# Kernel optimization log

Measured on AMD Instinct MI355X. Metric: run time of the kernel, lower is better.

## Reference

```python
import jax, jax.numpy as jnp
import numpy as np

N, D, H, T = 50000, 512, 512, 16
N_HOP = 1
NEG = -1e18


def setup_inputs() -> dict:
    key = jax.random.key(0)
    ks = jax.random.split(key, 16)
    s = 0.05  # param init scale
    inp = {
        "attn_mem": jax.random.normal(ks[0], (N, D), jnp.float32),
        "stop": jax.random.uniform(ks[1], (D,), jnp.float32, -0.01, 0.01),
        "init_h": jax.random.normal(ks[2], (H,), jnp.float32) * s,
        "init_c": jax.random.normal(ks[3], (H,), jnp.float32) * s,
        "init_i": jax.random.normal(ks[4], (D,), jnp.float32) * s,
        "attn_wm": jax.random.normal(ks[5], (D, H), jnp.float32) * s,
        "attn_wq": jax.random.normal(ks[6], (H, H), jnp.float32) * s,
        "attn_v": jax.random.normal(ks[7], (H,), jnp.float32) * s,
        "hop_wm": jax.random.normal(ks[8], (D, H), jnp.float32) * s,
        "hop_wq": jax.random.normal(ks[9], (H, H), jnp.float32) * s,
        "hop_v": jax.random.normal(ks[10], (H,), jnp.float32) * s,
        "w_ih": jax.random.normal(ks[11], (4 * H, D), jnp.float32) * s,
        "w_hh": jax.random.normal(ks[12], (4 * H, H), jnp.float32) * s,
        "b_ih": jax.random.normal(ks[13], (4 * H,), jnp.float32) * s,
        "b_hh": jax.random.normal(ks[14], (4 * H,), jnp.float32) * s,
        # precomputed gumbel noise -> categorical sampling via gumbel-max
        "gumbel": jax.random.gumbel(ks[15], (T, N + 1), jnp.float32),
    }
    return inp


def _attn_score(feat, q, v, w):
    # feat: [M, H], q: [H] -> unnormalized scores [M]
    return jnp.tanh(feat + q @ w) @ v


def reference(attn_mem, stop, init_h, init_c, init_i, attn_wm, attn_wq, attn_v,
              hop_wm, hop_wq, hop_v, w_ih, w_hh, b_ih, b_hh, gumbel):
    mem = jnp.concatenate([attn_mem, stop[None, :]], axis=0)  # [N+1, D]
    attn_feat = mem @ attn_wm                                  # [N+1, H]
    hop_feat = mem @ hop_wm                                    # [N+1, H]
    stop_idx = mem.shape[0] - 1

    def lstm_cell(x, h, c):
        gates = x @ w_ih.T + b_ih + h @ w_hh.T + b_hh          # [4H]
        i, f, g, o = jnp.split(gates, 4)
        i, f, o = jax.nn.sigmoid(i), jax.nn.sigmoid(f), jax.nn.sigmoid(o)
        c_new = f * c + i * jnp.tanh(g)
        return o * jnp.tanh(c_new), c_new

    def step(carry, g):
        h, c, x, sel, done = carry
        h, c = lstm_cell(x, h, c)
        q = h
        for _ in range(N_HOP):  # glimpse hops
            s = _attn_score(hop_feat, q, hop_v, hop_wq)
            q = jax.nn.softmax(s) @ hop_feat
        score = _attn_score(attn_feat, q, attn_v, attn_wq)     # [N+1]
        score = jnp.where(sel, NEG, score)                     # mask selected
        logp_all = jax.nn.log_softmax(score)
        out = jnp.argmax(score + g)                            # Categorical sample
        logp = jnp.where(done, 0.0, logp_all[out])
        out_rec = jnp.where(done, stop_idx, out)
        sel = jnp.where(done, sel, sel.at[out].set(True))
        new_done = done | (out == stop_idx)
        x = jnp.where(new_done, x, mem[out])
        return (h, c, x, sel, new_done), (out_rec.astype(jnp.int32), logp)

    carry0 = (init_h, init_c, init_i,
              jnp.zeros((mem.shape[0],), jnp.bool_), jnp.array(False))
    _, (outs, logps) = jax.lax.scan(step, carry0, gumbel)
    return outs, logps
```

## Files before the change

### kernel.cpp

```cpp
#include <hip/hip_runtime.h>
#include <math.h>

#define NITEMS 50000
#define NROWS 50001
#define NP 50176
#define DD 512
#define HH 512
#define TT 16
#define NEGV (-1e18f)
#define NGRP 784
#define NGC 196

typedef unsigned long long ull;
typedef unsigned short ushort;
typedef short short8 __attribute__((ext_vector_type(8)));
typedef float f32x4 __attribute__((ext_vector_type(4)));

#define AST(p, v) __hip_atomic_store((p), (v), __ATOMIC_RELAXED, __HIP_MEMORY_SCOPE_AGENT)
#define ALD(p) __hip_atomic_load((p), __ATOMIC_RELAXED, __HIP_MEMORY_SCOPE_AGENT)
#define AADD_REL(p) __hip_atomic_fetch_add((p), 1u, __ATOMIC_ACQ_REL, __HIP_MEMORY_SCOPE_AGENT)
#define FLAG_SET(p) __hip_atomic_store((p), 1u, __ATOMIC_RELEASE, __HIP_MEMORY_SCOPE_AGENT)
#define FLAG_GET(p) __hip_atomic_load((p), __ATOMIC_ACQUIRE, __HIP_MEMORY_SCOPE_AGENT)

__device__ __forceinline__ unsigned fkey(float f) {
  unsigned u = __float_as_uint(f);
  return (u & 0x80000000u) ? ~u : (u | 0x80000000u);
}
__device__ __forceinline__ float ftanh(float x) {
  float e = __builtin_amdgcn_exp2f(x * 2.885390081777927f);
  return 1.f - 2.f * __builtin_amdgcn_rcpf(e + 1.f);
}
__device__ __forceinline__ float fexp(float x) {
  return __builtin_amdgcn_exp2f(x * 1.4426950408889634f);
}
__device__ __forceinline__ ushort rne1(float a) {
  unsigned u = __float_as_uint(a);
  return (ushort)((u + 0x7fffu + ((u >> 16) & 1u)) >> 16);
}
__device__ __forceinline__ float bf2f(ushort h) { return __uint_as_float((unsigned)h << 16); }
__device__ __forceinline__ unsigned pack_bf16(float a, float b) {
  return (unsigned)rne1(a) | ((unsigned)rne1(b) << 16);
}
__device__ __forceinline__ float bflo(unsigned u) { return __uint_as_float(u << 16); }
__device__ __forceinline__ float bfhi(unsigned u) { return __uint_as_float(u & 0xffff0000u); }

__device__ __forceinline__ void gl_lds16(const void* g, void* l) {
#if __has_builtin(__builtin_amdgcn_global_load_lds)
  __builtin_amdgcn_global_load_lds((const __attribute__((address_space(1))) unsigned*)g,
                                   (__attribute__((address_space(3))) unsigned*)l, 16, 0, 0);
#else
  const int lane = threadIdx.x & 63;
  *(uint4*)((char*)l + lane * 16) = *(const uint4*)g;
#endif
}

#define MFMA(a, b, c) __builtin_amdgcn_mfma_f32_16x16x32_bf16(a, b, c, 0, 0, 0)

__global__ void k_convA(const float* __restrict__ A0, const float* __restrict__ stoprow,
                        ushort* __restrict__ Ahi, ushort* __restrict__ Alo,
                        int* __restrict__ sel, unsigned* __restrict__ cnts) {
  const size_t t = (size_t)blockIdx.x * 256 + threadIdx.x;
  if (blockIdx.x < 196) {
    int i = blockIdx.x * 256 + threadIdx.x;
    if (i < NROWS) sel[i] = 0;
    if (blockIdx.x == 0 && threadIdx.x < 128) cnts[threadIdx.x] = 0;
  }
  const size_t base = t * 8;
  const int row = (int)(base >> 9);
  float v[8];
  if (row < NITEMS) {
    const float4* p = (const float4*)(A0 + base);
    float4 x = p[0], y = p[1];
    v[0] = x.x; v[1] = x.y; v[2] = x.z; v[3] = x.w;
    v[4] = y.x; v[5] = y.y; v[6] = y.z; v[7] = y.w;
  } else if (row == NITEMS) {
    const float4* p = (const float4*)(stoprow + (base & 511));
    float4 x = p[0], y = p[1];
    v[0] = x.x; v[1] = x.y; v[2] = x.z; v[3] = x.w;
    v[4] = y.x; v[5] = y.y; v[6] = y.z; v[7] = y.w;
  } else {
#pragma unroll
    for (int j = 0; j < 8; ++j) v[j] = 0.f;
  }
  unsigned hw[4], lw[4];
#pragma unroll
  for (int j = 0; j < 4; ++j) {
    float a0 = v[2 * j], a1 = v[2 * j + 1];
    ushort h0 = rne1(a0), h1 = rne1(a1);
    hw[j] = (unsigned)h0 | ((unsigned)h1 << 16);
    lw[j] = pack_bf16(a0 - bf2f(h0), a1 - bf2f(h1));
  }
  *(uint4*)(Ahi + base) = make_uint4(hw[0], hw[1], hw[2], hw[3]);
  *(uint4*)(Alo + base) = make_uint4(lw[0], lw[1], lw[2], lw[3]);
}

__global__ void k_convBT2(const float* __restrict__ Wa, const float* __restrict__ Wh,
                          ushort* __restrict__ WhiT_a, ushort* __restrict__ WloT_a,
                          ushort* __restrict__ WhiT_h, ushort* __restrict__ WloT_h) {
  const int n = blockIdx.x & 511;
  const float* W = (blockIdx.x < 512) ? Wa : Wh;
  ushort* Whi = (blockIdx.x < 512) ? WhiT_a : WhiT_h;
  ushort* Wlo = (blockIdx.x < 512) ? WloT_a : WloT_h;
  const int k0 = threadIdx.x * 2;
  float a0 = W[(size_t)k0 * 512 + n];
  float a1 = W[(size_t)(k0 + 1) * 512 + n];
  ushort h0 = rne1(a0), h1 = rne1(a1);
  *(unsigned*)(Whi + (size_t)n * 512 + k0) = (unsigned)h0 | ((unsigned)h1 << 16);
  *(unsigned*)(Wlo + (size_t)n * 512 + k0) = pack_bf16(a0 - bf2f(h0), a1 - bf2f(h1));
}

__launch_bounds__(256, 2)
__global__ void k_mfma(const ushort* __restrict__ Ahi, const ushort* __restrict__ Alo,
                       const ushort* __restrict__ BhT, const ushort* __restrict__ BlT,
                       ushort* __restrict__ C) {
  __shared__ __align__(16) char lds[65536];
  char* sA0 = lds;
  char* sA1 = lds + 16384;
  char* sB0 = lds + 32768;
  char* sB1 = lds + 49152;
  const int tid = threadIdx.x;
  const int lane = tid & 63, w = tid >> 6;
  const int lid = blockIdx.y * 4 + blockIdx.x;
  const int xcd = lid & 7, pos = lid >> 3;
  const int orig = xcd * 196 + pos;
  const int m0 = (orig >> 2) * 128, n0 = (orig & 3) * 128;
  const int aR0 = (w & 1) * 64, bR0 = (w >> 1) * 64;

  f32x4 acc[4][4];
  const f32x4 z4 = {0.f, 0.f, 0.f, 0.f};
#pragma unroll
  for (int i = 0; i < 4; ++i)
#pragma unroll
    for (int j = 0; j < 4; ++j) acc[i][j] = z4;

#define STAGE_ALL(KT)                                                                     \
  {                                                                                       \
    _Pragma("unroll") for (int i = 0; i < 4; ++i) {                                       \
      const int row = i * 32 + (tid >> 3);                                                \
      const int kb = ((tid & 7) << 4) ^ ((row & 7) << 4);                                 \
      const int ldso = i * 4096 + (w << 10);                                              \
      gl_lds16((const char*)(Ahi + ((size_t)(m0 + row) << 9) + (KT)) + kb, sA0 + ldso);   \
      gl_lds16((const char*)(Alo + ((size_t)(m0 + row) << 9) + (KT)) + kb, sA1 + ldso);   \
      gl_lds16((const char*)(BhT + ((size_t)(n0 + row) << 9) + (KT)) + kb, sB0 + ldso);   \
      gl_lds16((const char*)(BlT + ((size_t)(n0 + row) << 9) + (KT)) + kb, sB1 + ldso);   \
    }                                                                                     \
  }

  STAGE_ALL(0)
  __syncthreads();
  for (int c = 0; c < 8; ++c) {
#pragma unroll
    for (int ks = 0; ks < 2; ++ks) {
      short8 ah[4], al[4], bh[4], bl[4];
      const int kbb = ks * 64 + ((lane >> 4) << 4);
#pragma unroll
      for (int f = 0; f < 4; ++f) {
        const int ra = aR0 + f * 16 + (lane & 15);
        const int oa = ra * 128 + (kbb ^ ((ra & 7) << 4));
        ah[f] = *(const short8*)(sA0 + oa);
        al[f] = *(const short8*)(sA1 + oa);
        const int rb = bR0 + f * 16 + (lane & 15);
        const int ob = rb * 128 + (kbb ^ ((rb & 7) << 4));
        bh[f] = *(const short8*)(sB0 + ob);
        bl[f] = *(const short8*)(sB1 + ob);
      }
#pragma unroll
      for (int mf = 0; mf < 4; ++mf)
#pragma unroll
        for (int nf = 0; nf < 4; ++nf) {
          acc[mf][nf] = MFMA(ah[mf], bh[nf], acc[mf][nf]);
          acc[mf][nf] = MFMA(ah[mf], bl[nf], acc[mf][nf]);
          acc[mf][nf] = MFMA(al[mf], bh[nf], acc[mf][nf]);
        }
    }
    if (c < 7) {
      __syncthreads();
      STAGE_ALL((c + 1) * 64)
      __syncthreads();
    }
  }
#undef STAGE_ALL

#pragma unroll
  for (int mf = 0; mf < 4; ++mf)
#pragma unroll
    for (int nf = 0; nf < 4; ++nf) {
      const f32x4 a = acc[mf][nf];
      const int n = n0 + bR0 + nf * 16 + (lane & 15);
      const int mb = m0 + aR0 + mf * 16 + ((lane >> 4) << 2);
      ushort* p = C + (size_t)n * NP + mb;
      *(uint2*)p = make_uint2(pack_bf16(a.x, a.y), pack_bf16(a.z, a.w));
    }
}

__launch_bounds__(256)
__global__ void k_A(const float* __restrict__ attn_mem, const float* __restrict__ stoprow,
                    const float* __restrict__ init_i, const float* __restrict__ init_h,
                    const float* __restrict__ init_c,
                    const float* __restrict__ w_ih, const float* __restrict__ w_hh,
                    const float* __restrict__ b_ih, const float* __restrict__ b_hh,
                    const float* __restrict__ hop_wq,
                    float* __restrict__ hv0, float* __restrict__ hv1,
                    float* __restrict__ cv0, float* __restrict__ cv1,
                    float* __restrict__ b1, const int* __restrict__ xrow_buf,
                    unsigned* __restrict__ cntA, unsigned* __restrict__ flagA, int t) {
  __shared__ float g4[4];
  __shared__ float hs[512];
  __shared__ float red2[256];
  __shared__ int sOld;
  const int b = blockIdx.x, tid = threadIdx.x, w = tid >> 6, lane = tid & 63;
  const int xrow = (t == 0) ? -1 : ALD((int*)xrow_buf);
  const float* xp = (xrow < 0) ? init_i
                               : ((xrow == NITEMS) ? stoprow : attn_mem + (size_t)xrow * DD);
  const float* hsrc = (t == 0) ? init_h : ((t & 1) ? hv0 : hv1);
  float* hdst = (t & 1) ? hv1 : hv0;
  const float* csrc = (t == 0) ? init_c : ((t & 1) ? cv0 : cv1);
  float* cdst = (t & 1) ? cv1 : cv0;

  const int r = w * 512 + b;
  const float4* x4 = (const float4*)xp;
  const float4* h4 = (const float4*)hsrc;
  const float4* wi = (const float4*)(w_ih + (size_t)r * DD);
  const float4* wh = (const float4*)(w_hh + (size_t)r * DD);
  float s = 0.f;
  float4 a, ww;
  a = x4[lane * 2];     ww = wi[lane * 2];     s += a.x * ww.x + a.y * ww.y + a.z * ww.z + a.w * ww.w;
  a = x4[lane * 2 + 1]; ww = wi[lane * 2 + 1]; s += a.x * ww.x + a.y * ww.y + a.z * ww.z + a.w * ww.w;
  a = h4[lane * 2];     ww = wh[lane * 2];     s += a.x * ww.x + a.y * ww.y + a.z * ww.z + a.w * ww.w;
  a = h4[lane * 2 + 1]; ww = wh[lane * 2 + 1]; s += a.x * ww.x + a.y * ww.y + a.z * ww.z + a.w * ww.w;
#pragma unroll
  for (int off = 32; off > 0; off >>= 1) s += __shfl_xor(s, off);
  if (lane == 0) g4[w] = s + b_ih[r] + b_hh[r];
  __syncthreads();
  if (tid == 0) {
    const float si = 1.f / (1.f + expf(-g4[0]));
    const float sf = 1.f / (1.f + expf(-g4[1]));
    const float so = 1.f / (1.f + expf(-g4[3]));
    const float cn = sf * csrc[b] + si * tanhf(g4[2]);
    cdst[b] = cn;
    AST(&hdst[b], so * tanhf(cn));
  }
  __syncthreads();
  if (tid == 0) {
    unsigned old = AADD_REL(cntA);
    if (old == 511u) { FLAG_SET(flagA); AST(cntA, 0u); }
    sOld = (int)old;
  }
  __syncthreads();
  const int old = sOld;
  if (old >= 496) {
    if (tid == 0 && old != 511) {
      while (FLAG_GET(flagA) == 0u) __builtin_amdgcn_s_sleep(2);
    }
    __syncthreads();
    const int c0 = (old - 496) * 32;
    hs[tid] = ALD(&hdst[tid]);
    hs[tid + 256] = ALD(&hdst[tid + 256]);
    __syncthreads();
    const int col = c0 + (tid & 31), seg = tid >> 5;
    float acc = 0.f;
#pragma unroll 8
    for (int i = seg * 64; i < seg * 64 + 64; ++i)
      acc = fmaf(hs[i], hop_wq[(size_t)i * 512 + col], acc);
    red2[tid] = acc;
    __syncthreads();
    if (tid < 32) {
      float sm = 0.f;
#pragma unroll
      for (int g2 = 0; g2 < 8; ++g2) sm += red2[tid + 32 * g2];
      b1[c0 + tid] = sm;
    }
  }
}

__launch_bounds__(512)
__global__ void k_B1(const ushort* __restrict__ featT, const float* __restrict__ b1v,
                     const float* __restrict__ hv, float* __restrict__ e,
                     float* __restrict__ bZ1, float* __restrict__ Zt,
                     unsigned* __restrict__ cntB1) {
  __shared__ float spart[8][256];
  __shared__ float rz[512];
  __shared__ int isLast;
  const int tid = threadIdx.x, g = blockIdx.x;
  const int w = tid >> 6, lane = tid & 63;
  const int mb = g * 256 + lane * 4;
  const int h0 = w * 64;
  const ushort* fp = featT + (size_t)h0 * NP + mb;
  float a0 = 0.f, a1 = 0.f, a2 = 0.f, a3 = 0.f;
#pragma unroll 8
  for (int hh = 0; hh < 64; ++hh) {
    const uint2 u = *(const uint2*)fp;
    fp += NP;
    const float bb = b1v[h0 + hh], vv = hv[h0 + hh];
    a0 += ftanh(bflo(u.x) + bb) * vv;
    a1 += ftanh(bfhi(u.x) + bb) * vv;
    a2 += ftanh(bflo(u.y) + bb) * vv;
    a3 += ftanh(bfhi(u.y) + bb) * vv;
  }
  spart[w][lane * 4 + 0] = a0;
  spart[w][lane * 4 + 1] = a1;
  spart[w][lane * 4 + 2] = a2;
  spart[w][lane * 4 + 3] = a3;
  __syncthreads();
  if (w < 4) {
    const int idx = w * 64 + lane;
    const int m = g * 256 + idx;
    float s = 0.f;
#pragma unroll
    for (int w2 = 0; w2 < 8; ++w2) s += spart[w2][idx];
    float ev = (m < NROWS) ? fexp(s) : 0.f;
    e[m] = ev;
    float Z = ev;
#pragma unroll
    for (int off = 32; off > 0; off >>= 1) Z += __shfl_xor(Z, off);
    if (lane == 0) AST(&bZ1[g * 4 + w], Z);
  }
  __syncthreads();
  if (tid == 0) {
    unsigned old = AADD_REL(cntB1);
    isLast = (old == gridDim.x - 1);
    if (isLast) AST(cntB1, 0u);
  }
  __syncthreads();
  if (isLast) {
    float Zl = 0.f;
    for (int i = tid; i < NGRP; i += 512) Zl += ALD(&bZ1[i]);
    rz[tid] = Zl;
    __syncthreads();
    for (int s2 = 256; s2 > 0; s2 >>= 1) {
      if (tid < s2) rz[tid] += rz[tid + s2];
      __syncthreads();
    }
    if (tid == 0) *Zt = rz[0];
  }
}

__launch_bounds__(256)
__global__ void k_B2(const ushort* __restrict__ featT, const float* __restrict__ e,
                     const float* __restrict__ Zt, const float* __restrict__ attn_wq,
                     float* __restrict__ qn, float* __restrict__ b2,
                     unsigned* __restrict__ cntB2, unsigned* __restrict__ flagB2) {
  __shared__ float red[256];
  __shared__ int sOld;
  const int tid = threadIdx.x, h = blockIdx.x;
  const ushort* fr = featT + (size_t)h * NP;
  float acc = 0.f;
#pragma unroll 4
  for (int m0 = tid * 8; m0 < NP; m0 += 2048) {
    const uint4 F = *(const uint4*)(fr + m0);
    const float4 e0 = *(const float4*)(e + m0);
    const float4 e1 = *(const float4*)(e + m0 + 4);
    acc += bflo(F.x) * e0.x + bfhi(F.x) * e0.y + bflo(F.y) * e0.z + bfhi(F.y) * e0.w +
           bflo(F.z) * e1.x + bfhi(F.z) * e1.y + bflo(F.w) * e1.z + bfhi(F.w) * e1.w;
  }
  red[tid] = acc;
  __syncthreads();
  for (int s2 = 128; s2 > 0; s2 >>= 1) {
    if (tid < s2) red[tid] += red[tid + s2];
    __syncthreads();
  }
  if (tid == 0) AST(&qn[h], red[0] / (*Zt));
  __syncthreads();
  if (tid == 0) {
    unsigned old = AADD_REL(cntB2);
    if (old == 511u) { FLAG_SET(flagB2); AST(cntB2, 0u); }
    sOld = (int)old;
  }
  __syncthreads();
  const int old = sOld;
  if (old >= 504) {
    const int li = old - 504;
    if (tid == 0 && old != 511) {
      while (FLAG_GET(flagB2) == 0u) __builtin_amdgcn_s_sleep(2);
    }
    __syncthreads();
    const int j = li * 64 + (tid & 63), is = tid >> 6;
    float a = 0.f;
#pragma unroll 8
    for (int i2 = is * 128; i2 < is * 128 + 128; ++i2)
      a = fmaf(ALD(&qn[i2]), attn_wq[(size_t)i2 * 512 + j], a);
    red[tid] = a;
    __syncthreads();
    if (tid < 64) b2[li * 64 + tid] = red[tid] + red[tid + 64] + red[tid + 128] + red[tid + 192];
  }
}

__launch_bounds__(512)
__global__ void k_C(const ushort* __restrict__ featT, const float* __restrict__ b2,
                    const float* __restrict__ av, int* __restrict__ sel,
                    const float* __restrict__ gum,
                    float* __restrict__ bZa, ull* __restrict__ bkey, float* __restrict__ bsc,
                    int* __restrict__ done_buf, int* __restrict__ xrow_buf,
                    float* __restrict__ outf, unsigned* __restrict__ cntC, int t) {
  __shared__ float spart[8][256];
  __shared__ float rz[512];
  __shared__ ull rk[512];
  __shared__ float rs[512];
  __shared__ int isLast;
  const int tid = threadIdx.x, g = blockIdx.x;
  const int w = tid >> 6, lane = tid & 63;
  const int mb = g * 256 + lane * 4;
  const int h0 = w * 64;
  const ushort* fp = featT + (size_t)h0 * NP + mb;
  float a0 = 0.f, a1 = 0.f, a2 = 0.f, a3 = 0.f;
#pragma unroll 8
  for (int hh = 0; hh < 64; ++hh) {
    const uint2 u = *(const uint2*)fp;
    fp += NP;
    const float bb = b2[h0 + hh], vv = av[h0 + hh];
    a0 += ftanh(bflo(u.x) + bb) * vv;
    a1 += ftanh(bfhi(u.x) + bb) * vv;
    a2 += ftanh(bflo(u.y) + bb) * vv;
    a3 += ftanh(bfhi(u.y) + bb) * vv;
  }
  spart[w][lane * 4 + 0] = a0;
  spart[w][lane * 4 + 1] = a1;
  spart[w][lane * 4 + 2] = a2;
  spart[w][lane * 4 + 3] = a3;
  __syncthreads();
  if (w < 4) {
    const int idx = w * 64 + lane;
    const int m = g * 256 + idx;
    float s = 0.f;
#pragma unroll
    for (int w2 = 0; w2 < 8; ++w2) s += spart[w2][idx];
    const bool valid = (m < NROWS);
    float Z, sv;
    ull key;
    if (valid) {
      const float se = sel[m] ? NEGV : s;
      sv = se;
      key = ((ull)fkey(se + gum[m]) << 32) | (unsigned)(NITEMS - m);
      Z = fexp(se);
    } else {
      key = 0;
      Z = 0.f;
      sv = 0.f;
    }
#pragma unroll
    for (int off = 32; off > 0; off >>= 1) {
      Z += __shfl_xor(Z, off);
      ull Ko = __shfl_xor(key, off);
      float so = __shfl_xor(sv, off);
      if (Ko > key) { key = Ko; sv = so; }
    }
    if (lane == 0) {
      AST(&bZa[g * 4 + w], Z);
      AST(&bkey[g * 4 + w], key);
      AST(&bsc[g * 4 + w], sv);
    }
  }
  __syncthreads();
  if (tid == 0) {
    unsigned old = AADD_REL(cntC);
    isLast = (old == gridDim.x - 1);
    if (isLast) AST(cntC, 0u);
  }
  __syncthreads();
  if (isLast) {
    float Zl = 0.f, Sl = 0.f;
    ull Kl = 0;
    for (int i = tid; i < NGRP; i += 512) {
      Zl += ALD(&bZa[i]);
      ull k = ALD(&bkey[i]);
      if (k > Kl) { Kl = k; Sl = ALD(&bsc[i]); }
    }
    rz[tid] = Zl;
    rk[tid] = Kl;
    rs[tid] = Sl;
    __syncthreads();
    for (int s2 = 256; s2 > 0; s2 >>= 1) {
      if (tid < s2) {
        rz[tid] += rz[tid + s2];
        if (rk[tid + s2] > rk[tid]) { rk[tid] = rk[tid + s2]; rs[tid] = rs[tid + s2]; }
      }
      __syncthreads();
    }
    if (tid == 0) {
      const float Z = rz[0];
      const ull K = rk[0];
      const int out = NITEMS - (int)(unsigned)(K & 0xffffffffull);
      const int d_in = (t == 0) ? 0 : *done_buf;
      const int xprev = (t == 0) ? -1 : *xrow_buf;
      const int nd = d_in | (out == NITEMS);
      outf[t] = (float)(d_in ? NITEMS : out);
      outf[TT + t] = d_in ? 0.f : (rs[0] - logf(Z));
      if (!d_in) sel[out] = 1;
      *done_buf = nd;
      *xrow_buf = nd ? xprev : out;
    }
  }
}

extern "C" void kernel_launch(void* const* d_in, const int* in_sizes, int n_in,
                              void* d_out, int out_size, void* d_ws, size_t ws_size,
                              hipStream_t stream) {
  const float* attn_mem = (const float*)d_in[0];
  const float* stoprow  = (const float*)d_in[1];
  const float* init_h   = (const float*)d_in[2];
  const float* init_c   = (const float*)d_in[3];
  const float* init_i   = (const float*)d_in[4];
  const float* attn_wm  = (const float*)d_in[5];
  const float* attn_wq  = (const float*)d_in[6];
  const float* attn_v   = (const float*)d_in[7];
  const float* hop_wm   = (const float*)d_in[8];
  const float* hop_wq   = (const float*)d_in[9];
  const float* hop_v    = (const float*)d_in[10];
  const float* w_ih     = (const float*)d_in[11];
  const float* w_hh     = (const float*)d_in[12];
  const float* b_ih     = (const float*)d_in[13];
  const float* b_hh     = (const float*)d_in[14];
  const float* gumbel   = (const float*)d_in[15];

  float* ws = (float*)d_ws;
  size_t fo = 0;
  const size_t FB = (size_t)NP * 512 / 2;
  ushort* hop_featT  = (ushort*)(ws + fo); fo += FB;
  ushort* attn_featT = (ushort*)(ws + fo); fo += FB;
  ushort* Ahi = (ushort*)(ws + fo); fo += FB;
  ushort* Alo = (ushort*)(ws + fo); fo += FB;
  ushort* WhiT_a = (ushort*)(ws + fo); fo += 131072;
  ushort* WloT_a = (ushort*)(ws + fo); fo += 131072;
  ushort* WhiT_h = (ushort*)(ws + fo); fo += 131072;
  ushort* WloT_h = (ushort*)(ws + fo); fo += 131072;
  int* sel   = (int*)(ws + fo); fo += NP;
  float* e   = ws + fo; fo += NP;
  float* bZ1 = ws + fo; fo += 1024;
  float* bZa = ws + fo; fo += 1024;
  float* bsc = ws + fo; fo += 1024;
  ull* bkey  = (ull*)(ws + fo); fo += 2048;
  float* hv0 = ws + fo; fo += HH;
  float* hv1 = ws + fo; fo += HH;
  float* cv0 = ws + fo; fo += HH;
  float* cv1 = ws + fo; fo += HH;
  float* b1  = ws + fo; fo += HH;
  float* b2  = ws + fo; fo += HH;
  float* qn  = ws + fo; fo += HH;
  float* Ztp = ws + fo; fo += 2;
  unsigned* cnts = (unsigned*)(ws + fo); fo += 128;
  int* done_buf = (int*)(ws + fo); fo += 2;
  int* xrow_buf = (int*)(ws + fo); fo += 2;
  if (fo * sizeof(float) > ws_size) return;

  float* outf = (float*)d_out;

  k_convA<<<(NP * 512 / 8) / 256, 256, 0, stream>>>(attn_mem, stoprow, Ahi, Alo, sel, cnts);
  k_convBT2<<<1024, 256, 0, stream>>>(attn_wm, hop_wm, WhiT_a, WloT_a, WhiT_h, WloT_h);

  dim3 ggrid(4, NP / 128);
  k_mfma<<<ggrid, 256, 0, stream>>>(Ahi, Alo, WhiT_a, WloT_a, attn_featT);
  k_mfma<<<ggrid, 256, 0, stream>>>(Ahi, Alo, WhiT_h, WloT_h, hop_featT);

  for (int t = 0; t < TT; ++t) {
    k_A<<<512, 256, 0, stream>>>(attn_mem, stoprow, init_i, init_h, init_c,
                                 w_ih, w_hh, b_ih, b_hh, hop_wq,
                                 hv0, hv1, cv0, cv1, b1, xrow_buf,
                                 cnts + 0, cnts + 16 + t, t);
    k_B1<<<NGC, 512, 0, stream>>>(hop_featT, b1, hop_v, e, bZ1, Ztp, cnts + 1);
    k_B2<<<512, 256, 0, stream>>>(hop_featT, e, Ztp, attn_wq, qn, b2,
                                  cnts + 3, cnts + 32 + t);
    k_C<<<NGC, 512, 0, stream>>>(attn_featT, b2, attn_v, sel,
                                 gumbel + (size_t)t * NROWS, bZa, bkey, bsc,
                                 done_buf, xrow_buf, outf, cnts + 2, t);
  }
}
```

Measured before the change: 1.627 ms.

## Fuse hop-attention score and glimpse reduction into one kernel with per-block partials

Merges k_B1 and k_B2 into a single kernel. Each block keeps its exp scores in LDS and immediately computes partial glimpse sums over its own 256-row tile of hop_featT, writing per-block partial vectors. The last 16 blocks to arrive then reduce the partials, normalize by Z, and compute b2 = q·attn_wq. This removes one launch per step and the second full pass over hop_featT and e, at the cost of a partial buffer, extra spin-waits, and a strided re-read of the block's feature tile.

```diff
diff --git a/kernel.cpp b/kernel.cpp
--- a/kernel.cpp
+++ b/kernel.cpp
@@ -274,114 +274,129 @@
 }
 
 __launch_bounds__(512)
-__global__ void k_B1(const ushort* __restrict__ featT, const float* __restrict__ b1v,
-                     const float* __restrict__ hv, float* __restrict__ e,
-                     float* __restrict__ bZ1, float* __restrict__ Zt,
-                     unsigned* __restrict__ cntB1) {
+__global__ void k_B(const ushort* __restrict__ featT, const float* __restrict__ b1v,
+                    const float* __restrict__ hv, const float* __restrict__ attn_wq,
+                    float* __restrict__ qp, float* __restrict__ bZ1,
+                    float* __restrict__ qn, float* __restrict__ b2,
+                    unsigned* __restrict__ cnt1, unsigned* __restrict__ cnt2,
+                    unsigned* __restrict__ flagQ, unsigned* __restrict__ flagB2) {
   __shared__ float spart[8][256];
-  __shared__ float rz[512];
-  __shared__ int isLast;
+  __shared__ float e_lds[256];
+  __shared__ float red[512];
+  __shared__ int sOld;
   const int tid = threadIdx.x, g = blockIdx.x;
   const int w = tid >> 6, lane = tid & 63;
-  const int mb = g * 256 + lane * 4;
-  const int h0 = w * 64;
-  const ushort* fp = featT + (size_t)h0 * NP + mb;
-  float a0 = 0.f, a1 = 0.f, a2 = 0.f, a3 = 0.f;
+  const int mb0 = g * 256;
+
+  {
+    const int mb = mb0 + lane * 4;
+    const int h0 = w * 64;
+    const ushort* fp = featT + (size_t)h0 * NP + mb;
+    float a0 = 0.f, a1 = 0.f, a2 = 0.f, a3 = 0.f;
 #pragma unroll 8
-  for (int hh = 0; hh < 64; ++hh) {
-    const uint2 u = *(const uint2*)fp;
-    fp += NP;
-    const float bb = b1v[h0 + hh], vv = hv[h0 + hh];
-    a0 += ftanh(bflo(u.x) + bb) * vv;
-    a1 += ftanh(bfhi(u.x) + bb) * vv;
-    a2 += ftanh(bflo(u.y) + bb) * vv;
-    a3 += ftanh(bfhi(u.y) + bb) * vv;
-  }
-  spart[w][lane * 4 + 0] = a0;
-  spart[w][lane * 4 + 1] = a1;
-  spart[w][lane * 4 + 2] = a2;
-  spart[w][lane * 4 + 3] = a3;
+    for (int hh = 0; hh < 64; ++hh) {
+      const uint2 u = *(const uint2*)fp;
+      fp += NP;
+      const float bb = b1v[h0 + hh], vv = hv[h0 + hh];
+      a0 += ftanh(bflo(u.x) + bb) * vv;
+      a1 += ftanh(bfhi(u.x) + bb) * vv;
+      a2 += ftanh(bflo(u.y) + bb) * vv;
+      a3 += ftanh(bfhi(u.y) + bb) * vv;
+    }
+    spart[w][lane * 4 + 0] = a0;
+    spart[w][lane * 4 + 1] = a1;
+    spart[w][lane * 4 + 2] = a2;
+    spart[w][lane * 4 + 3] = a3;
+  }
   __syncthreads();
   if (w < 4) {
     const int idx = w * 64 + lane;
-    const int m = g * 256 + idx;
+    const int m = mb0 + idx;
     float s = 0.f;
 #pragma unroll
     for (int w2 = 0; w2 < 8; ++w2) s += spart[w2][idx];
     float ev = (m < NROWS) ? fexp(s) : 0.f;
-    e[m] = ev;
+    e_lds[idx] = ev;
     float Z = ev;
 #pragma unroll
     for (int off = 32; off > 0; off >>= 1) Z += __shfl_xor(Z, off);
     if (lane == 0) AST(&bZ1[g * 4 + w], Z);
   }
   __syncthreads();
+
+  {
+    const ushort* fr = featT + (size_t)tid * NP + mb0;
+    float acc = 0.f;
+#pragma unroll 4
+    for (int j = 0; j < 256; j += 8) {
+      const uint4 F = *(const uint4*)(fr + j);
+      acc += bflo(F.x) * e_lds[j + 0] + bfhi(F.x) * e_lds[j + 1] +
+             bflo(F.y) * e_lds[j + 2] + bfhi(F.y) * e_lds[j + 3] +
+             bflo(F.z) * e_lds[j + 4] + bfhi(F.z) * e_lds[j + 5] +
+             bflo(F.w) * e_lds[j + 6] + bfhi(F.w) * e_lds[j + 7];
+    }
+    AST(&qp[(size_t)g * 512 + tid], acc);
+  }
+  __syncthreads();
+
   if (tid == 0) {
-    unsigned old = AADD_REL(cntB1);
-    isLast = (old == gridDim.x - 1);
-    if (isLast) AST(cntB1, 0u);
-  }
-  __syncthreads();
-  if (isLast) {
-    float Zl = 0.f;
-    for (int i = tid; i < NGRP; i += 512) Zl += ALD(&bZ1[i]);
-    rz[tid] = Zl;
+    unsigned old = AADD_REL(cnt1);
+    if (old == NGC - 1u) { FLAG_SET(flagQ); AST(cnt1, 0u); }
+    sOld = (int)old;
+  }
+  __syncthreads();
+  const int old = sOld;
+  if (old >= NGC - 16) {
+    if (tid == 0 && old != NGC - 1) {
+      while (FLAG_GET(flagQ) == 0u) __builtin_amdgcn_s_sleep(2);
+    }
+    __syncthreads();
+    float zl = 0.f;
+    for (int i = tid; i < NGRP; i += 512) zl += ALD(&bZ1[i]);
+    red[tid] = zl;
     __syncthreads();
     for (int s2 = 256; s2 > 0; s2 >>= 1) {
-      if (tid < s2) rz[tid] += rz[tid + s2];
+      if (tid < s2) red[tid] += red[tid + s2];
       __syncthreads();
     }
-    if (tid == 0) *Zt = rz[0];
-  }
-}
-
-__launch_bounds__(256)
-__global__ void k_B2(const ushort* __restrict__ featT, const float* __restrict__ e,
-                     const float* __restrict__ Zt, const float* __restrict__ attn_wq,
-                     float* __restrict__ qn, float* __restrict__ b2,
-                     unsigned* __restrict__ cntB2, unsigned* __restrict__ flagB2) {
-  __shared__ float red[256];
-  __shared__ int sOld;
-  const int tid = threadIdx.x, h = blockIdx.x;
-  const ushort* fr = featT + (size_t)h * NP;
-  float acc = 0.f;
-#pragma unroll 4
-  for (int m0 = tid * 8; m0 < NP; m0 += 2048) {
-    const uint4 F = *(const uint4*)(fr + m0);
-    const float4 e0 = *(const float4*)(e + m0);
-    const float4 e1 = *(const float4*)(e + m0 + 4);
-    acc += bflo(F.x) * e0.x + bfhi(F.x) * e0.y + bflo(F.y) * e0.z + bfhi(F.y) * e0.w +
-           bflo(F.z) * e1.x + bfhi(F.z) * e1.y + bflo(F.w) * e1.z + bfhi(F.w) * e1.w;
-  }
-  red[tid] = acc;
-  __syncthreads();
-  for (int s2 = 128; s2 > 0; s2 >>= 1) {
-    if (tid < s2) red[tid] += red[tid + s2];
-    __syncthreads();
-  }
-  if (tid == 0) AST(&qn[h], red[0] / (*Zt));
-  __syncthreads();
-  if (tid == 0) {
-    unsigned old = AADD_REL(cntB2);
-    if (old == 511u) { FLAG_SET(flagB2); AST(cntB2, 0u); }
-    sOld = (int)old;
-  }
-  __syncthreads();
-  const int old = sOld;
-  if (old >= 504) {
-    const int li = old - 504;
-    if (tid == 0 && old != 511) {
-      while (FLAG_GET(flagB2) == 0u) __builtin_amdgcn_s_sleep(2);
-    }
-    __syncthreads();
-    const int j = li * 64 + (tid & 63), is = tid >> 6;
-    float a = 0.f;
+    const float Zt = red[0];
+    __syncthreads();
+    const int li = old - (NGC - 16);
+    {
+      const int h = li * 32 + (tid & 31), seg = tid >> 5;
+      float a = 0.f;
+      for (int g2 = seg; g2 < NGC; g2 += 16) a += ALD(&qp[(size_t)g2 * 512 + h]);
+      red[tid] = a;
+      __syncthreads();
+      if (tid < 32) {
+        float sm = 0.f;
+#pragma unroll
+        for (int s2 = 0; s2 < 16; ++s2) sm += red[tid + 32 * s2];
+        AST(&qn[li * 32 + tid], sm / Zt);
+      }
+    }
+    __syncthreads();
+    if (tid == 0) {
+      unsigned o2 = AADD_REL(cnt2);
+      if (o2 == 15u) { FLAG_SET(flagB2); AST(cnt2, 0u); }
+      else { while (FLAG_GET(flagB2) == 0u) __builtin_amdgcn_s_sleep(2); }
+    }
+    __syncthreads();
+    {
+      const int j = li * 32 + (tid & 31), seg = tid >> 5;
+      float a = 0.f;
 #pragma unroll 8
-    for (int i2 = is * 128; i2 < is * 128 + 128; ++i2)
-      a = fmaf(ALD(&qn[i2]), attn_wq[(size_t)i2 * 512 + j], a);
-    red[tid] = a;
-    __syncthreads();
-    if (tid < 64) b2[li * 64 + tid] = red[tid] + red[tid + 64] + red[tid + 128] + red[tid + 192];
+      for (int i2 = seg * 32; i2 < seg * 32 + 32; ++i2)
+        a = fmaf(ALD(&qn[i2]), attn_wq[(size_t)i2 * 512 + j], a);
+      red[tid] = a;
+      __syncthreads();
+      if (tid < 32) {
+        float sm = 0.f;
+#pragma unroll
+        for (int s2 = 0; s2 < 16; ++s2) sm += red[tid + 32 * s2];
+        b2[li * 32 + tid] = sm;
+      }
+    }
   }
 }
 
@@ -524,7 +539,7 @@
   ushort* WhiT_h = (ushort*)(ws + fo); fo += 131072;
   ushort* WloT_h = (ushort*)(ws + fo); fo += 131072;
   int* sel   = (int*)(ws + fo); fo += NP;
-  float* e   = ws + fo; fo += NP;
+  float* qp  = ws + fo; fo += (size_t)NGC * 512;
   float* bZ1 = ws + fo; fo += 1024;
   float* bZa = ws + fo; fo += 1024;
   float* bsc = ws + fo; fo += 1024;
@@ -536,7 +551,6 @@
   float* b1  = ws + fo; fo += HH;
   float* b2  = ws + fo; fo += HH;
   float* qn  = ws + fo; fo += HH;
-  float* Ztp = ws + fo; fo += 2;
   unsigned* cnts = (unsigned*)(ws + fo); fo += 128;
   int* done_buf = (int*)(ws + fo); fo += 2;
   int* xrow_buf = (int*)(ws + fo); fo += 2;
@@ -555,10 +569,9 @@
     k_A<<<512, 256, 0, stream>>>(attn_mem, stoprow, init_i, init_h, init_c,
                                  w_ih, w_hh, b_ih, b_hh, hop_wq,
                                  hv0, hv1, cv0, cv1, b1, xrow_buf,
-                                 cnts + 0, cnts + 16 + t, t);
-    k_B1<<<NGC, 512, 0, stream>>>(hop_featT, b1, hop_v, e, bZ1, Ztp, cnts + 1);
-    k_B2<<<512, 256, 0, stream>>>(hop_featT, e, Ztp, attn_wq, qn, b2,
-                                  cnts + 3, cnts + 32 + t);
+                                 cnts + 0, cnts + 48 + t, t);
+    k_B<<<NGC, 512, 0, stream>>>(hop_featT, b1, hop_v, attn_wq, qp, bZ1, qn, b2,
+                                 cnts + 1, cnts + 3, cnts + 16 + t, cnts + 32 + t);
     k_C<<<NGC, 512, 0, stream>>>(attn_featT, b2, attn_v, sel,
                                  gumbel + (size_t)t * NROWS, bZa, bkey, bsc,
                                  done_buf, xrow_buf, outf, cnts + 2, t);
```

Result: faster. 1.370 ms (-15.8%).
